# Optimization experiments

Hardware: AMD Instinct MI355X
Metric: run time of the kernel (lower is better)

Reference implementation:

```python
import jax, jax.numpy as jnp
import numpy as np

N = 100000      # nodes
E = 1600000     # edges
F_IN = 64       # num_node_features
R = 8           # num_relations
G = 256         # graphs in batch
H, C = 4, 32    # GAT heads, per-head channels
NEG_SLOPE_ATT = 0.2    # GATConv attention leaky relu
NEG_SLOPE = 0.01       # F.leaky_relu default


def setup_inputs() -> dict:
    key = jax.random.key(0)
    ks = jax.random.split(key, 12)
    init = lambda k, shape, fan: (jax.random.normal(k, shape, jnp.float32) / np.sqrt(fan).astype(np.float32))
    x = jax.random.normal(ks[0], (N, F_IN), jnp.float32)
    edge_index = jax.random.randint(ks[1], (2, E), 0, N)
    edge_type = jax.random.randint(ks[2], (E,), 0, R)
    batch = (jnp.arange(N) * G) // N  # sorted graph ids, every segment non-empty
    return dict(
        x=x, edge_index=edge_index, edge_type=edge_type, batch=batch,
        gat_w=init(ks[3], (F_IN, H * C), F_IN),
        gat_att_src=init(ks[4], (H, C), C),
        gat_att_dst=init(ks[5], (H, C), C),
        gat_bias=jnp.zeros((H * C,), jnp.float32),
        dense1_w=init(ks[6], (H * C, 16), H * C),
        dense1_b=jnp.zeros((16,), jnp.float32),
        rw1=init(ks[7], (R, F_IN, 32), F_IN),
        root1=init(ks[8], (F_IN, 32), F_IN),
        rb1=jnp.zeros((32,), jnp.float32),
        rw2=init(ks[9], (R, 32, 16), 32),
        root2=init(ks[10], (32, 16), 32),
        rb2=jnp.zeros((16,), jnp.float32),
        dense_w=init(ks[11], (32, 1), 32),
        dense_b=jnp.zeros((1,), jnp.float32),
    )


def _gat(x, src, dst, w, att_src, att_dst, bias):
    h = (x @ w).reshape(N, H, C)                       # [N,H,C]
    a_src = jnp.sum(h * att_src, axis=-1)              # [N,H]
    a_dst = jnp.sum(h * att_dst, axis=-1)              # [N,H]
    e = jax.nn.leaky_relu(a_src[src] + a_dst[dst], NEG_SLOPE_ATT)  # [E,H]
    # segment softmax over incoming edges of each dst node
    m = jax.ops.segment_max(e, dst, num_segments=N)    # [N,H]
    p = jnp.exp(e - m[dst])
    s = jax.ops.segment_sum(p, dst, num_segments=N)    # [N,H]
    alpha = p / s[dst]
    msg = h[src] * alpha[:, :, None]                   # [E,H,C]
    out = jax.ops.segment_sum(msg, dst, num_segments=N)
    return out.reshape(N, H * C) + bias


def _rgcn(x, src, dst, edge_type, w, root, bias):
    # per-relation transform of all nodes, then edge gather (PyG RGCNConv, aggr='mean')
    xw = jnp.einsum('ni,rio->rno', x, w)               # [R,N,out]
    msg = xw[edge_type, src]                           # [E,out]
    comb = dst * R + edge_type                         # mean is per (dst, relation)
    cnt = jax.ops.segment_sum(jnp.ones((E,), x.dtype), comb, num_segments=N * R)
    agg = jax.ops.segment_sum(msg / cnt[comb][:, None], dst, num_segments=N)
    return agg + x @ root + bias


def reference(x, edge_index, edge_type, batch, gat_w, gat_att_src, gat_att_dst,
              gat_bias, dense1_w, dense1_b, rw1, root1, rb1, rw2, root2, rb2,
              dense_w, dense_b):
    src, dst = edge_index[0], edge_index[1]
    # GAT branch (dropout treated as identity / eval mode)
    h = _gat(x, src, dst, gat_w, gat_att_src, gat_att_dst, gat_bias)
    h = jax.nn.leaky_relu(h, NEG_SLOPE)
    h = jax.nn.leaky_relu(h @ dense1_w + dense1_b, NEG_SLOPE)
    gmax = jax.ops.segment_max(h, batch, num_segments=G)          # [G,16]
    # RGCN branch
    z = jax.nn.relu(_rgcn(x, src, dst, edge_type, rw1, root1, rb1))
    z = jax.nn.relu(_rgcn(z, src, dst, edge_type, rw2, root2, rb2))
    nodes_per_graph = jax.ops.segment_sum(jnp.ones((N,), x.dtype), batch, num_segments=G)
    gmean = jax.ops.segment_sum(z, batch, num_segments=G) / nodes_per_graph[:, None]
    # fuse
    zc = jnp.concatenate([gmax, gmean], axis=1)                   # [G,32]
    return zc @ dense_w + dense_b                                  # [G,1]
```

## Files before the change

### kernel.cpp

```cpp
#include <hip/hip_runtime.h>
#include <hip/hip_bf16.h>

typedef __hip_bfloat16 bf16;
typedef unsigned short u16;

#define N_NODES 100000
#define N_EDGES 1600000
#define F_IN 64
#define N_REL 8
#define N_GRAPH 256
#define N_HEAD 4
#define HC 128
#define NBLK_SCAN 391

__device__ __forceinline__ float lrelu(float x, float s) { return x >= 0.f ? x : s * x; }
__device__ __forceinline__ unsigned fenc(float f) {
  unsigned b = __float_as_uint(f);
  return (b & 0x80000000u) ? ~b : (b | 0x80000000u);
}
__device__ __forceinline__ float fdec(unsigned u) {
  float v = __uint_as_float((u & 0x80000000u) ? (u & 0x7fffffffu) : ~u);
  return fmaxf(fminf(v, 3e38f), -3e38f);
}
__device__ __forceinline__ float bf2f(bf16 v) { return __bfloat162float(v); }
__device__ __forceinline__ bf16 f2bf(float v) { return __float2bfloat16(v); }
__device__ __forceinline__ float lo_bf(unsigned u) { return __uint_as_float(u << 16); }
__device__ __forceinline__ float hi_bf(unsigned u) { return __uint_as_float(u & 0xFFFF0000u); }
__device__ __forceinline__ unsigned f2bfu(float v) {
  unsigned u = __float_as_uint(v);
  return (u + 0x7FFFu + ((u >> 16) & 1u)) >> 16;
}

template<bool BF> __device__ __forceinline__ float ldf(const void* p, size_t i) {
  if (BF) { u16 v = ((const u16*)p)[i]; return __uint_as_float(((unsigned)v) << 16); }
  else    { return ((const float*)p)[i]; }
}
template<bool BF> __device__ __forceinline__ float2 ldf2(const void* p, size_t i) {
  if (BF) { unsigned v = ((const unsigned*)p)[i]; return make_float2(lo_bf(v), hi_bf(v)); }
  else    { return ((const float2*)p)[i]; }
}

__global__ void k_probe(const u16* __restrict__ xr, int* __restrict__ flag) {
  int t = threadIdx.x;
  int c = 0;
  for (int i = t; i < 1024; i += 256) {
    unsigned e = (xr[i] >> 7) & 0xFFu;
    if (e >= 100u && e <= 140u) c++;
  }
  __shared__ int sc[256];
  sc[t] = c;
  __syncthreads();
  for (int s = 128; s; s >>= 1) { if (t < s) sc[t] += sc[t + s]; __syncthreads(); }
  if (t == 0) *flag = (sc[0] >= 800) ? 1 : 0;
}

template<bool BF>
__device__ __forceinline__ void gat_h_body(const void* x, const void* w, const void* att_s,
                                           const void* att_d, u16* __restrict__ h,
                                           float* __restrict__ a_src, float* __restrict__ a_dst,
                                           int n, float* xs) {
  int j = threadIdx.x;
  if (j < F_IN) xs[j] = ldf<BF>(x, (size_t)n * F_IN + j);
  __syncthreads();
  float acc = 0.f;
#pragma unroll
  for (int k = 0; k < F_IN; ++k) acc += xs[k] * ldf<BF>(w, (size_t)k * HC + j);
  h[(size_t)n * HC + j] = (u16)f2bfu(acc);
  float ps = acc * ldf<BF>(att_s, j);
  float pd = acc * ldf<BF>(att_d, j);
#pragma unroll
  for (int off = 16; off > 0; off >>= 1) {
    ps += __shfl_down(ps, off, 32);
    pd += __shfl_down(pd, off, 32);
  }
  if ((j & 31) == 0) {
    a_src[n * N_HEAD + (j >> 5)] = ps;
    a_dst[n * N_HEAD + (j >> 5)] = pd;
  }
}

__global__ void k_gath_hist(const void* x, const void* w, const void* att_s, const void* att_d,
                            u16* h, float* a_src, float* a_dst,
                            const int* __restrict__ ei, const int* __restrict__ etype,
                            int* __restrict__ deg, int* __restrict__ cnt, const int* flag) {
  __shared__ float xs[F_IN];
  if (blockIdx.x < N_NODES) {
    if (__builtin_amdgcn_readfirstlane(*flag))
      gat_h_body<true>(x, w, att_s, att_d, h, a_src, a_dst, blockIdx.x, xs);
    else
      gat_h_body<false>(x, w, att_s, att_d, h, a_src, a_dst, blockIdx.x, xs);
  } else {
    int e = (blockIdx.x - N_NODES) * 128 + threadIdx.x;
    if (e < N_EDGES) {
      int d = ei[N_EDGES + e], t = etype[e];
      atomicAdd(&deg[d], 1);
      atomicAdd(&cnt[d * N_REL + t], 1);
    }
  }
}

__global__ void k_scan_a(const int* __restrict__ deg, int* __restrict__ rowptr,
                         int* __restrict__ scanblk) {
  __shared__ int buf[256];
  int tid = threadIdx.x;
  int i = blockIdx.x * 256 + tid;
  int v = (i < N_NODES) ? deg[i] : 0;
  buf[tid] = v;
  __syncthreads();
  for (int st = 1; st < 256; st <<= 1) {
    int t = buf[tid];
    int a = (tid >= st) ? buf[tid - st] : 0;
    __syncthreads();
    buf[tid] = t + a;
    __syncthreads();
  }
  if (i < N_NODES) rowptr[i] = buf[tid] - v;
  if (tid == 255) scanblk[blockIdx.x] = buf[255];
}
__global__ void k_scan_b(int* __restrict__ scanblk) {
  __shared__ int buf[512];
  int tid = threadIdx.x;
  int v = (tid < NBLK_SCAN) ? scanblk[tid] : 0;
  buf[tid] = v;
  __syncthreads();
  for (int st = 1; st < 512; st <<= 1) {
    int t = buf[tid];
    int a = (tid >= st) ? buf[tid - st] : 0;
    __syncthreads();
    buf[tid] = t + a;
    __syncthreads();
  }
  if (tid < NBLK_SCAN) scanblk[tid] = buf[tid] - v;
}
__global__ void k_scan_c(int* __restrict__ rowptr, int* __restrict__ wp,
                         const int* __restrict__ scanblk) {
  int i = blockIdx.x * 256 + threadIdx.x;
  if (i < N_NODES) {
    int val = rowptr[i] + scanblk[blockIdx.x];
    rowptr[i] = val;
    wp[i] = val;
  } else if (i == N_NODES) {
    rowptr[N_NODES] = N_EDGES;
  }
}

__global__ void k_scatter(const int* __restrict__ ei, const int* __restrict__ etype,
                          const float* __restrict__ a_src, const float* __restrict__ a_dst,
                          int* __restrict__ wp, unsigned* __restrict__ csr,
                          float4* __restrict__ p_logit, int* __restrict__ dstarr) {
  int e = blockIdx.x * 256 + threadIdx.x;
  if (e >= N_EDGES) return;
  int sn = ei[e], d = ei[N_EDGES + e], t = etype[e];
  int pos = atomicAdd(&wp[d], 1);
  csr[pos] = (unsigned)sn | ((unsigned)t << 20);
  dstarr[pos] = d;
  const float4 as = *(const float4*)&a_src[sn * 4];
  const float4 ad = *(const float4*)&a_dst[d * 4];
  float4 lg;
  lg.x = lrelu(as.x + ad.x, 0.2f);
  lg.y = lrelu(as.y + ad.y, 0.2f);
  lg.z = lrelu(as.z + ad.z, 0.2f);
  lg.w = lrelu(as.w + ad.w, 0.2f);
  p_logit[pos] = lg;
}

__global__ void k_msum(const int* __restrict__ rowptr, const float* __restrict__ p_logit,
                       float* __restrict__ m_arr, float* __restrict__ si_arr) {
  int tid = threadIdx.x;
  int n = blockIdx.x * 16 + (tid >> 4);
  int l16 = tid & 15, head = l16 & 3, slot = l16 >> 2;
  int base = rowptr[n], deg = rowptr[n + 1] - base;
  float m = -1e30f;
  for (int i = slot; i < deg; i += 4) m = fmaxf(m, p_logit[(size_t)(base + i) * 4 + head]);
  m = fmaxf(m, __shfl_xor(m, 4, 64));
  m = fmaxf(m, __shfl_xor(m, 8, 64));
  float s = 0.f;
  for (int i = slot; i < deg; i += 4) s += __expf(p_logit[(size_t)(base + i) * 4 + head] - m);
  s += __shfl_xor(s, 4, 64);
  s += __shfl_xor(s, 8, 64);
  if (slot == 0) {
    m_arr[n * 4 + head] = m;
    si_arr[n * 4 + head] = (deg > 0) ? 1.f / s : 0.f;
  }
}

__global__ void k_alpha(const int* __restrict__ dstarr, const float* __restrict__ m_arr,
                        const float* __restrict__ si_arr, float4* __restrict__ plog4) {
  int p = blockIdx.x * 256 + threadIdx.x;
  if (p >= N_EDGES) return;
  int d = dstarr[p];
  float4 lg = plog4[p];
  const float4 m4 = *(const float4*)&m_arr[d * 4];
  const float4 s4 = *(const float4*)&si_arr[d * 4];
  float4 a;
  a.x = __expf(lg.x - m4.x) * s4.x;
  a.y = __expf(lg.y - m4.y) * s4.y;
  a.z = __expf(lg.z - m4.z) * s4.z;
  a.w = __expf(lg.w - m4.w) * s4.w;
  plog4[p] = a;
}

template<bool BF>
__device__ __forceinline__ void gat_agg_body(const int* __restrict__ rowptr,
                                             const unsigned* __restrict__ csr,
                                             const float* __restrict__ alpha,
                                             const uint2* __restrict__ hu2, const void* gbias,
                                             const void* d1w, const void* d1b,
                                             const int* __restrict__ batch,
                                             unsigned* __restrict__ gmax, int* __restrict__ npg,
                                             float (*os)[132], int bid) {
  int tid = threadIdx.x;
  int wave = tid >> 6, l = tid & 63;
  int d = bid * 4 + wave;
  int base = rowptr[d];
  int deg = rowptr[d + 1] - base;
  int slot = l >> 5, cl = l & 31;
  int head = cl >> 3;
  float a0 = 0.f, a1 = 0.f, a2 = 0.f, a3 = 0.f;
  int i = slot;
  for (; i + 6 < deg; i += 8) {
    unsigned sp0 = csr[base + i],     sp1 = csr[base + i + 2];
    unsigned sp2 = csr[base + i + 4], sp3 = csr[base + i + 6];
    float av0 = alpha[(size_t)(base + i) * 4 + head];
    float av1 = alpha[(size_t)(base + i + 2) * 4 + head];
    float av2 = alpha[(size_t)(base + i + 4) * 4 + head];
    float av3 = alpha[(size_t)(base + i + 6) * 4 + head];
    uint2 h0 = hu2[(size_t)(sp0 & 0xFFFFF) * 32 + cl];
    uint2 h1 = hu2[(size_t)(sp1 & 0xFFFFF) * 32 + cl];
    uint2 h2 = hu2[(size_t)(sp2 & 0xFFFFF) * 32 + cl];
    uint2 h3 = hu2[(size_t)(sp3 & 0xFFFFF) * 32 + cl];
    a0 += lo_bf(h0.x) * av0 + lo_bf(h1.x) * av1 + lo_bf(h2.x) * av2 + lo_bf(h3.x) * av3;
    a1 += hi_bf(h0.x) * av0 + hi_bf(h1.x) * av1 + hi_bf(h2.x) * av2 + hi_bf(h3.x) * av3;
    a2 += lo_bf(h0.y) * av0 + lo_bf(h1.y) * av1 + lo_bf(h2.y) * av2 + lo_bf(h3.y) * av3;
    a3 += hi_bf(h0.y) * av0 + hi_bf(h1.y) * av1 + hi_bf(h2.y) * av2 + hi_bf(h3.y) * av3;
  }
  for (; i < deg; i += 2) {
    unsigned sp = csr[base + i];
    float av = alpha[(size_t)(base + i) * 4 + head];
    uint2 hv = hu2[(size_t)(sp & 0xFFFFF) * 32 + cl];
    a0 += lo_bf(hv.x) * av;
    a1 += hi_bf(hv.x) * av;
    a2 += lo_bf(hv.y) * av;
    a3 += hi_bf(hv.y) * av;
  }
  a0 += __shfl_xor(a0, 32, 64);
  a1 += __shfl_xor(a1, 32, 64);
  a2 += __shfl_xor(a2, 32, 64);
  a3 += __shfl_xor(a3, 32, 64);
  if (slot == 0) {
    os[wave][4 * cl + 0] = lrelu(a0 + ldf<BF>(gbias, 4 * cl + 0), 0.01f);
    os[wave][4 * cl + 1] = lrelu(a1 + ldf<BF>(gbias, 4 * cl + 1), 0.01f);
    os[wave][4 * cl + 2] = lrelu(a2 + ldf<BF>(gbias, 4 * cl + 2), 0.01f);
    os[wave][4 * cl + 3] = lrelu(a3 + ldf<BF>(gbias, 4 * cl + 3), 0.01f);
  }
  __syncthreads();
  if (tid < 64) {
    int node = tid >> 4, out = tid & 15;
    float acc = ldf<BF>(d1b, out);
#pragma unroll
    for (int k = 0; k < HC; ++k) acc += os[node][k] * ldf<BF>(d1w, (size_t)k * 16 + out);
    acc = lrelu(acc, 0.01f);
    atomicMax(&gmax[batch[bid * 4 + node] * 16 + out], fenc(acc));
  }
  if (tid < 4) atomicAdd(&npg[batch[bid * 4 + tid]], 1);
}

template<bool BF>
__device__ __forceinline__ void xw1_body(const void* x, const void* rw1, bf16* __restrict__ xw1,
                                         int n0, int r, float (*xs)[F_IN]) {
  int tid = threadIdx.x;
  for (int i = tid; i < 8 * F_IN; i += 256) {
    int nn = n0 + (i >> 6);
    xs[i >> 6][i & 63] = (nn < N_NODES) ? ldf<BF>(x, (size_t)nn * F_IN + (i & 63)) : 0.f;
  }
  __syncthreads();
  int nl = tid >> 5, c = tid & 31;
  int n = n0 + nl;
  float acc = 0.f;
#pragma unroll
  for (int k = 0; k < F_IN; ++k) acc += xs[nl][k] * ldf<BF>(rw1, (size_t)(r * F_IN + k) * 32 + c);
  if (n < N_NODES) xw1[((size_t)r * N_NODES + n) * 32 + c] = f2bf(acc);
}

__global__ void k_aggxw1(const int* rowptr, const unsigned* csr, const float* alpha,
                         const u16* h, const void* gbias, const void* d1w, const void* d1b,
                         const int* batch, unsigned* gmax, int* npg,
                         const void* x, const void* rw1, bf16* xw1, const int* flag) {
  __shared__ float sh[544];
  int bf = __builtin_amdgcn_readfirstlane(*flag);
  if (blockIdx.x < 25000) {
    if (bf) gat_agg_body<true>(rowptr, csr, alpha, (const uint2*)h, gbias, d1w, d1b,
                               batch, gmax, npg, (float(*)[132])sh, blockIdx.x);
    else    gat_agg_body<false>(rowptr, csr, alpha, (const uint2*)h, gbias, d1w, d1b,
                                batch, gmax, npg, (float(*)[132])sh, blockIdx.x);
  } else {
    int nb = blockIdx.x - 25000;
    int n0 = (nb % 12500) * 8;
    int r  = nb / 12500;
    if (bf) xw1_body<true>(x, rw1, xw1, n0, r, (float(*)[F_IN])sh);
    else    xw1_body<false>(x, rw1, xw1, n0, r, (float(*)[F_IN])sh);
  }
}

template<bool BF>
__device__ __forceinline__ void ragg1_body(const int* __restrict__ rowptr,
                                           const unsigned* __restrict__ csr,
                                           const int* __restrict__ cnt,
                                           const unsigned* __restrict__ xw, const void* x,
                                           const void* root1, const void* rb1,
                                           float* __restrict__ z1) {
  __shared__ float xs[4][F_IN];
  __shared__ float cinv[4][N_REL];
  int tid = threadIdx.x;
  int n0 = blockIdx.x * 4;
  {
    int nn = n0 + (tid >> 6);
    xs[tid >> 6][tid & 63] = ldf<BF>(x, (size_t)nn * F_IN + (tid & 63));
  }
  if (tid < 32) {
    int cv = cnt[(n0 + (tid >> 3)) * N_REL + (tid & 7)];
    cinv[tid >> 3][tid & 7] = (cv > 0) ? 1.f / (float)cv : 0.f;
  }
  __syncthreads();
  int wave = tid >> 6, l = tid & 63;
  int slot = l >> 4, cl = l & 15;
  int n = n0 + wave;
  int base = rowptr[n], deg = rowptr[n + 1] - base;
  float a0 = 0.f, a1 = 0.f;
  int i = slot;
  for (; i + 4 < deg; i += 8) {
    unsigned sp0 = csr[base + i], sp1 = csr[base + i + 4];
    int t0 = sp0 >> 20, t1 = sp1 >> 20;
    unsigned v0 = xw[((size_t)t0 * N_NODES + (sp0 & 0xFFFFF)) * 16 + cl];
    unsigned v1 = xw[((size_t)t1 * N_NODES + (sp1 & 0xFFFFF)) * 16 + cl];
    float c0 = cinv[wave][t0], c1 = cinv[wave][t1];
    a0 += lo_bf(v0) * c0 + lo_bf(v1) * c1;
    a1 += hi_bf(v0) * c0 + hi_bf(v1) * c1;
  }
  if (i < deg) {
    unsigned sp = csr[base + i];
    int t = sp >> 20;
    unsigned v = xw[((size_t)t * N_NODES + (sp & 0xFFFFF)) * 16 + cl];
    float c0 = cinv[wave][t];
    a0 += lo_bf(v) * c0;
    a1 += hi_bf(v) * c0;
  }
#pragma unroll
  for (int kk = 0; kk < 16; ++kk) {
    int k = slot * 16 + kk;
    float xv = xs[wave][k];
    float2 wv = ldf2<BF>(root1, (size_t)k * 16 + cl);
    a0 += xv * wv.x;
    a1 += xv * wv.y;
  }
  a0 += __shfl_xor(a0, 16, 64); a0 += __shfl_xor(a0, 32, 64);
  a1 += __shfl_xor(a1, 16, 64); a1 += __shfl_xor(a1, 32, 64);
  if (slot == 0) {
    z1[(size_t)n * 32 + 2 * cl]     = fmaxf(a0 + ldf<BF>(rb1, 2 * cl), 0.f);
    z1[(size_t)n * 32 + 2 * cl + 1] = fmaxf(a1 + ldf<BF>(rb1, 2 * cl + 1), 0.f);
  }
}
__global__ void k_ragg1(const int* rowptr, const unsigned* csr, const int* cnt,
                        const bf16* xw1, const void* x, const void* root1, const void* rb1,
                        float* z1, const int* flag) {
  if (__builtin_amdgcn_readfirstlane(*flag))
    ragg1_body<true>(rowptr, csr, cnt, (const unsigned*)xw1, x, root1, rb1, z1);
  else
    ragg1_body<false>(rowptr, csr, cnt, (const unsigned*)xw1, x, root1, rb1, z1);
}

template<bool BF>
__device__ __forceinline__ void zw2_body(const float* __restrict__ z1, const void* rw2,
                                         bf16* __restrict__ zw2) {
  __shared__ float zs[16][32];
  int tid = threadIdx.x;
  int n0 = blockIdx.x * 16;
  for (int i = tid; i < 16 * 32; i += 256) {
    int nn = n0 + (i >> 5);
    zs[i >> 5][i & 31] = (nn < N_NODES) ? z1[(size_t)nn * 32 + (i & 31)] : 0.f;
  }
  __syncthreads();
  int nl = tid >> 4, c = tid & 15;
  int n = n0 + nl, r = blockIdx.y;
  float acc = 0.f;
#pragma unroll
  for (int k = 0; k < 32; ++k) acc += zs[nl][k] * ldf<BF>(rw2, (size_t)(r * 32 + k) * 16 + c);
  if (n < N_NODES) zw2[((size_t)r * N_NODES + n) * 16 + c] = f2bf(acc);
}
__global__ void k_zw2(const float* z1, const void* rw2, bf16* zw2, const int* flag) {
  if (__builtin_amdgcn_readfirstlane(*flag)) zw2_body<true>(z1, rw2, zw2);
  else zw2_body<false>(z1, rw2, zw2);
}

template<bool BF>
__device__ __forceinline__ void ragg2_body(const int* __restrict__ rowptr,
                                           const unsigned* __restrict__ csr,
                                           const int* __restrict__ cnt,
                                           const unsigned* __restrict__ zw,
                                           const float* __restrict__ z1, const void* root2,
                                           const void* rb2, const int* __restrict__ batch,
                                           float* __restrict__ gsum) {
  __shared__ float zs[4][33];
  __shared__ float cinv[4][N_REL];
  int tid = threadIdx.x;
  int n0 = blockIdx.x * 4;
  if (tid < 128) {
    int nn = n0 + (tid >> 5);
    zs[tid >> 5][tid & 31] = z1[(size_t)nn * 32 + (tid & 31)];
  }
  if (tid < 32) {
    int cv = cnt[(n0 + (tid >> 3)) * N_REL + (tid & 7)];
    cinv[tid >> 3][tid & 7] = (cv > 0) ? 1.f / (float)cv : 0.f;
  }
  __syncthreads();
  int wave = tid >> 6, l = tid & 63;
  int slot = l >> 3, cl = l & 7;
  int n = n0 + wave;
  int base = rowptr[n], deg = rowptr[n + 1] - base;
  float a0 = 0.f, a1 = 0.f;
  int i = slot;
  for (; i + 8 < deg; i += 16) {
    unsigned sp0 = csr[base + i], sp1 = csr[base + i + 8];
    int t0 = sp0 >> 20, t1 = sp1 >> 20;
    unsigned v0 = zw[((size_t)t0 * N_NODES + (sp0 & 0xFFFFF)) * 8 + cl];
    unsigned v1 = zw[((size_t)t1 * N_NODES + (sp1 & 0xFFFFF)) * 8 + cl];
    float c0 = cinv[wave][t0], c1 = cinv[wave][t1];
    a0 += lo_bf(v0) * c0 + lo_bf(v1) * c1;
    a1 += hi_bf(v0) * c0 + hi_bf(v1) * c1;
  }
  if (i < deg) {
    unsigned sp = csr[base + i];
    int t = sp >> 20;
    unsigned v = zw[((size_t)t * N_NODES + (sp & 0xFFFFF)) * 8 + cl];
    float c0 = cinv[wave][t];
    a0 += lo_bf(v) * c0;
    a1 += hi_bf(v) * c0;
  }
#pragma unroll
  for (int kk = 0; kk < 4; ++kk) {
    int k = slot * 4 + kk;
    float zv = zs[wave][k];
    float2 wv = ldf2<BF>(root2, (size_t)k * 8 + cl);
    a0 += zv * wv.x;
    a1 += zv * wv.y;
  }
  a0 += __shfl_xor(a0, 8, 64); a0 += __shfl_xor(a0, 16, 64); a0 += __shfl_xor(a0, 32, 64);
  a1 += __shfl_xor(a1, 8, 64); a1 += __shfl_xor(a1, 16, 64); a1 += __shfl_xor(a1, 32, 64);
  if (slot == 0) {
    float z2a = fmaxf(a0 + ldf<BF>(rb2, 2 * cl), 0.f);
    float z2b = fmaxf(a1 + ldf<BF>(rb2, 2 * cl + 1), 0.f);
    int g = batch[n];
    atomicAdd(&gsum[g * 16 + 2 * cl], z2a);
    atomicAdd(&gsum[g * 16 + 2 * cl + 1], z2b);
  }
}
__global__ void k_ragg2(const int* rowptr, const unsigned* csr, const int* cnt,
                        const bf16* zw2, const float* z1, const void* root2, const void* rb2,
                        const int* batch, float* gsum, const int* flag) {
  if (__builtin_amdgcn_readfirstlane(*flag))
    ragg2_body<true>(rowptr, csr, cnt, (const unsigned*)zw2, z1, root2, rb2, batch, gsum);
  else
    ragg2_body<false>(rowptr, csr, cnt, (const unsigned*)zw2, z1, root2, rb2, batch, gsum);
}

template<bool BF>
__device__ __forceinline__ void final_body(const unsigned* __restrict__ gmax,
                                           const float* __restrict__ gsum,
                                           const int* __restrict__ npg, const void* dw,
                                           const void* db, void* out) {
  int g = threadIdx.x;
  if (g >= N_GRAPH) return;
  float acc = ldf<BF>(db, 0);
  int np = npg[g]; if (np < 1) np = 1;
  float inv = 1.f / (float)np;
#pragma unroll
  for (int c = 0; c < 16; ++c) {
    acc += fdec(gmax[g * 16 + c]) * ldf<BF>(dw, c);
    acc += (gsum[g * 16 + c] * inv) * ldf<BF>(dw, 16 + c);
  }
  if (BF) ((bf16*)out)[g] = f2bf(acc);
  else ((float*)out)[g] = acc;
}
__global__ void k_final(const unsigned* gmax, const float* gsum, const int* npg,
                        const void* dw, const void* db, void* out, const int* flag) {
  if (__builtin_amdgcn_readfirstlane(*flag)) final_body<true>(gmax, gsum, npg, dw, db, out);
  else final_body<false>(gmax, gsum, npg, dw, db, out);
}

extern "C" void kernel_launch(void* const* d_in, const int* in_sizes, int n_in,
                              void* d_out, int out_size, void* d_ws, size_t ws_size,
                              hipStream_t stream) {
  const void* x        = d_in[0];
  const int*  ei       = (const int*)d_in[1];
  const int*  etype    = (const int*)d_in[2];
  const int*  batch    = (const int*)d_in[3];
  const void* gat_w    = d_in[4];
  const void* att_src  = d_in[5];
  const void* att_dst  = d_in[6];
  const void* gat_bias = d_in[7];
  const void* d1w      = d_in[8];
  const void* d1b      = d_in[9];
  const void* rw1      = d_in[10];
  const void* root1    = d_in[11];
  const void* rb1      = d_in[12];
  const void* rw2      = d_in[13];
  const void* root2    = d_in[14];
  const void* rb2      = d_in[15];
  const void* dw       = d_in[16];
  const void* db       = d_in[17];

  char* ws = (char*)d_ws;
  const size_t o_h     = 0;
  const size_t o_plog  = 25600000;
  const size_t o_xw1   = 51200000;
  const size_t o_dst   = 51200000;
  const size_t o_zw2   = 0;
  const size_t o_asrc  = 102400000;
  const size_t o_adst  = 104000000;
  const size_t o_deg   = 105600000;
  const size_t o_rowp  = 106000000;
  const size_t o_wp    = 106400016;
  const size_t o_cnt   = 106800016;
  const size_t o_csr   = 110000016;
  const size_t o_z1    = 116400016;
  const size_t o_sblk  = 129200016;
  const size_t o_gmax  = 129201600;
  const size_t o_gsum  = 129217984;
  const size_t o_npg   = 129234368;
  const size_t o_flag  = 129235392;
  const size_t total   = 129235396;
  if (ws_size < total) return;

  u16*      h      = (u16*)(ws + o_h);
  float*    plog   = (float*)(ws + o_plog);
  bf16*     xw1    = (bf16*)(ws + o_xw1);
  int*      dstarr = (int*)(ws + o_dst);
  bf16*     zw2    = (bf16*)(ws + o_zw2);
  float*    a_src  = (float*)(ws + o_asrc);
  float*    a_dst  = (float*)(ws + o_adst);
  int*      deg    = (int*)(ws + o_deg);
  int*      rowptr = (int*)(ws + o_rowp);
  int*      wp     = (int*)(ws + o_wp);
  int*      cnt    = (int*)(ws + o_cnt);
  unsigned* csr    = (unsigned*)(ws + o_csr);
  float*    z1     = (float*)(ws + o_z1);
  int*      sblk   = (int*)(ws + o_sblk);
  unsigned* gmax   = (unsigned*)(ws + o_gmax);
  float*    gsum   = (float*)(ws + o_gsum);
  int*      npg    = (int*)(ws + o_npg);
  int*      flag   = (int*)(ws + o_flag);

  k_probe<<<1, 256, 0, stream>>>((const u16*)x, flag);

  hipMemsetAsync(ws + o_deg, 0, o_csr - o_deg, stream);
  hipMemsetAsync(ws + o_gmax, 0, 33792, stream);

  k_gath_hist<<<N_NODES + 12500, 128, 0, stream>>>(x, gat_w, att_src, att_dst, h, a_src, a_dst,
                                                   ei, etype, deg, cnt, flag);

  k_scan_a<<<NBLK_SCAN, 256, 0, stream>>>(deg, rowptr, sblk);
  k_scan_b<<<1, 512, 0, stream>>>(sblk);
  k_scan_c<<<NBLK_SCAN, 256, 0, stream>>>(rowptr, wp, sblk);
  k_scatter<<<(N_EDGES + 255) / 256, 256, 0, stream>>>(ei, etype, a_src, a_dst, wp, csr,
                                                       (float4*)plog, dstarr);

  k_msum<<<N_NODES / 16, 256, 0, stream>>>(rowptr, plog, a_src, a_dst);
  k_alpha<<<(N_EDGES + 255) / 256, 256, 0, stream>>>(dstarr, a_src, a_dst, (float4*)plog);

  k_aggxw1<<<25000 + 100000, 256, 0, stream>>>(rowptr, csr, plog, h, gat_bias, d1w, d1b,
                                               batch, gmax, npg, x, rw1, xw1, flag);

  k_ragg1<<<N_NODES / 4, 256, 0, stream>>>(rowptr, csr, cnt, xw1, x, root1, rb1, z1, flag);

  k_zw2<<<dim3((N_NODES + 15) / 16, N_REL), 256, 0, stream>>>(z1, rw2, zw2, flag);
  k_ragg2<<<N_NODES / 4, 256, 0, stream>>>(rowptr, csr, cnt, zw2, z1, root2, rb2,
                                           batch, gsum, flag);

  k_final<<<1, 256, 0, stream>>>(gmax, gsum, npg, dw, db, d_out, flag);
}
```

Baseline: 1.232 ms.

## Fuse softmax into GAT aggregation and register-tile node transforms

The per-edge max/sum and alpha kernels are removed. Each wave now computes the segment max and inverse sum itself and applies exp on the fly while aggregating, which drops the dstarr array and a full pass over the logits. The GAT and x·rw1 transforms are register-tiled so each block handles 16 nodes with weights held in registers, and they are launched alongside the degree histogram. The RGCN layer-1 aggregation is merged into the GAT aggregation launch. The cost is that logits are read twice more inside the aggregation and each edge's exp is recomputed per channel lane.

```diff
diff --git a/kernel.cpp b/kernel.cpp
--- a/kernel.cpp
+++ b/kernel.cpp
@@ -55,47 +55,106 @@
 }
 
 template<bool BF>
-__device__ __forceinline__ void gat_h_body(const void* x, const void* w, const void* att_s,
-                                           const void* att_d, u16* __restrict__ h,
-                                           float* __restrict__ a_src, float* __restrict__ a_dst,
-                                           int n, float* xs) {
-  int j = threadIdx.x;
-  if (j < F_IN) xs[j] = ldf<BF>(x, (size_t)n * F_IN + j);
-  __syncthreads();
-  float acc = 0.f;
-#pragma unroll
-  for (int k = 0; k < F_IN; ++k) acc += xs[k] * ldf<BF>(w, (size_t)k * HC + j);
-  h[(size_t)n * HC + j] = (u16)f2bfu(acc);
-  float ps = acc * ldf<BF>(att_s, j);
-  float pd = acc * ldf<BF>(att_d, j);
-#pragma unroll
-  for (int off = 16; off > 0; off >>= 1) {
-    ps += __shfl_down(ps, off, 32);
-    pd += __shfl_down(pd, off, 32);
-  }
-  if ((j & 31) == 0) {
-    a_src[n * N_HEAD + (j >> 5)] = ps;
-    a_dst[n * N_HEAD + (j >> 5)] = pd;
-  }
-}
-
-__global__ void k_gath_hist(const void* x, const void* w, const void* att_s, const void* att_d,
-                            u16* h, float* a_src, float* a_dst,
-                            const int* __restrict__ ei, const int* __restrict__ etype,
-                            int* __restrict__ deg, int* __restrict__ cnt, const int* flag) {
-  __shared__ float xs[F_IN];
-  if (blockIdx.x < N_NODES) {
+__device__ __forceinline__ void gat_body(const void* x, const void* w, const void* att_s,
+                                         const void* att_d, u16* __restrict__ h,
+                                         float* __restrict__ a_src, float* __restrict__ a_dst,
+                                         int n0, float* xs) {
+  int tid = threadIdx.x;
+  for (int i = tid; i < 16 * F_IN; i += 256)
+    xs[i] = ldf<BF>(x, (size_t)(n0 + (i >> 6)) * F_IN + (i & 63));
+  __syncthreads();
+  int g = tid >> 7, c = tid & 127;
+  float as_c = ldf<BF>(att_s, c), ad_c = ldf<BF>(att_d, c);
+  float acc[8] = {0.f, 0.f, 0.f, 0.f, 0.f, 0.f, 0.f, 0.f};
+  for (int kh = 0; kh < F_IN; kh += 32) {
+    float wreg[32];
+#pragma unroll
+    for (int j = 0; j < 32; ++j) wreg[j] = ldf<BF>(w, (size_t)(kh + j) * HC + c);
+#pragma unroll
+    for (int n = 0; n < 8; ++n) {
+      const float* xr = &xs[(g * 8 + n) * F_IN + kh];
+#pragma unroll
+      for (int j = 0; j < 32; j += 4) {
+        float4 xv = *(const float4*)&xr[j];
+        acc[n] += xv.x * wreg[j];
+        acc[n] += xv.y * wreg[j + 1];
+        acc[n] += xv.z * wreg[j + 2];
+        acc[n] += xv.w * wreg[j + 3];
+      }
+    }
+  }
+  int l = tid & 63, head = c >> 5;
+#pragma unroll
+  for (int n = 0; n < 8; ++n) {
+    int node = n0 + g * 8 + n;
+    h[(size_t)node * HC + c] = (u16)f2bfu(acc[n]);
+    float ps = acc[n] * as_c, pd = acc[n] * ad_c;
+#pragma unroll
+    for (int off = 16; off > 0; off >>= 1) {
+      ps += __shfl_xor(ps, off, 64);
+      pd += __shfl_xor(pd, off, 64);
+    }
+    if ((l & 31) == 0) {
+      a_src[node * N_HEAD + head] = ps;
+      a_dst[node * N_HEAD + head] = pd;
+    }
+  }
+}
+
+template<bool BF>
+__device__ __forceinline__ void xw1_body(const void* x, const void* rw1, bf16* __restrict__ xw1,
+                                         int n0, float* xs) {
+  int tid = threadIdx.x;
+  for (int i = tid; i < 16 * F_IN; i += 256)
+    xs[i] = ldf<BF>(x, (size_t)(n0 + (i >> 6)) * F_IN + (i & 63));
+  __syncthreads();
+  int r = tid >> 5, c = tid & 31;
+  float acc[16] = {0.f, 0.f, 0.f, 0.f, 0.f, 0.f, 0.f, 0.f,
+                   0.f, 0.f, 0.f, 0.f, 0.f, 0.f, 0.f, 0.f};
+  for (int kh = 0; kh < F_IN; kh += 32) {
+    float wreg[32];
+#pragma unroll
+    for (int j = 0; j < 32; ++j)
+      wreg[j] = ldf<BF>(rw1, (size_t)(r * F_IN + kh + j) * 32 + c);
+#pragma unroll
+    for (int n = 0; n < 16; ++n) {
+      const float* xr = &xs[n * F_IN + kh];
+#pragma unroll
+      for (int j = 0; j < 32; j += 4) {
+        float4 xv = *(const float4*)&xr[j];
+        acc[n] += xv.x * wreg[j];
+        acc[n] += xv.y * wreg[j + 1];
+        acc[n] += xv.z * wreg[j + 2];
+        acc[n] += xv.w * wreg[j + 3];
+      }
+    }
+  }
+#pragma unroll
+  for (int n = 0; n < 16; ++n)
+    xw1[((size_t)r * N_NODES + (n0 + n)) * 32 + c] = f2bf(acc[n]);
+}
+
+__global__ void k_gxh(const void* x, const void* w, const void* att_s, const void* att_d,
+                      u16* h, float* a_src, float* a_dst, const void* rw1, bf16* xw1,
+                      const int* __restrict__ ei, const int* __restrict__ etype,
+                      int* __restrict__ deg, int* __restrict__ cnt, const int* flag) {
+  __shared__ __align__(16) float xs[16 * F_IN];
+  int bid = blockIdx.x;
+  if (bid < 6250) {
+    int e = bid * 256 + threadIdx.x;
+    int d = ei[N_EDGES + e], t = etype[e];
+    atomicAdd(&deg[d], 1);
+    atomicAdd(&cnt[d * N_REL + t], 1);
+  } else if (bid < 12500) {
+    int n0 = (bid - 6250) * 16;
     if (__builtin_amdgcn_readfirstlane(*flag))
-      gat_h_body<true>(x, w, att_s, att_d, h, a_src, a_dst, blockIdx.x, xs);
+      gat_body<true>(x, w, att_s, att_d, h, a_src, a_dst, n0, xs);
     else
-      gat_h_body<false>(x, w, att_s, att_d, h, a_src, a_dst, blockIdx.x, xs);
+      gat_body<false>(x, w, att_s, att_d, h, a_src, a_dst, n0, xs);
   } else {
-    int e = (blockIdx.x - N_NODES) * 128 + threadIdx.x;
-    if (e < N_EDGES) {
-      int d = ei[N_EDGES + e], t = etype[e];
-      atomicAdd(&deg[d], 1);
-      atomicAdd(&cnt[d * N_REL + t], 1);
-    }
+    int n0 = (bid - 12500) * 16;
+    if (__builtin_amdgcn_readfirstlane(*flag)) xw1_body<true>(x, rw1, xw1, n0, xs);
+    else xw1_body<false>(x, rw1, xw1, n0, xs);
   }
 }
 
@@ -147,13 +206,12 @@
 __global__ void k_scatter(const int* __restrict__ ei, const int* __restrict__ etype,
                           const float* __restrict__ a_src, const float* __restrict__ a_dst,
                           int* __restrict__ wp, unsigned* __restrict__ csr,
-                          float4* __restrict__ p_logit, int* __restrict__ dstarr) {
+                          float4* __restrict__ p_logit) {
   int e = blockIdx.x * 256 + threadIdx.x;
   if (e >= N_EDGES) return;
   int sn = ei[e], d = ei[N_EDGES + e], t = etype[e];
   int pos = atomicAdd(&wp[d], 1);
   csr[pos] = (unsigned)sn | ((unsigned)t << 20);
-  dstarr[pos] = d;
   const float4 as = *(const float4*)&a_src[sn * 4];
   const float4 ad = *(const float4*)&a_dst[d * 4];
   float4 lg;
@@ -164,67 +222,49 @@
   p_logit[pos] = lg;
 }
 
-__global__ void k_msum(const int* __restrict__ rowptr, const float* __restrict__ p_logit,
-                       float* __restrict__ m_arr, float* __restrict__ si_arr) {
-  int tid = threadIdx.x;
-  int n = blockIdx.x * 16 + (tid >> 4);
-  int l16 = tid & 15, head = l16 & 3, slot = l16 >> 2;
-  int base = rowptr[n], deg = rowptr[n + 1] - base;
-  float m = -1e30f;
-  for (int i = slot; i < deg; i += 4) m = fmaxf(m, p_logit[(size_t)(base + i) * 4 + head]);
-  m = fmaxf(m, __shfl_xor(m, 4, 64));
-  m = fmaxf(m, __shfl_xor(m, 8, 64));
-  float s = 0.f;
-  for (int i = slot; i < deg; i += 4) s += __expf(p_logit[(size_t)(base + i) * 4 + head] - m);
-  s += __shfl_xor(s, 4, 64);
-  s += __shfl_xor(s, 8, 64);
-  if (slot == 0) {
-    m_arr[n * 4 + head] = m;
-    si_arr[n * 4 + head] = (deg > 0) ? 1.f / s : 0.f;
-  }
-}
-
-__global__ void k_alpha(const int* __restrict__ dstarr, const float* __restrict__ m_arr,
-                        const float* __restrict__ si_arr, float4* __restrict__ plog4) {
-  int p = blockIdx.x * 256 + threadIdx.x;
-  if (p >= N_EDGES) return;
-  int d = dstarr[p];
-  float4 lg = plog4[p];
-  const float4 m4 = *(const float4*)&m_arr[d * 4];
-  const float4 s4 = *(const float4*)&si_arr[d * 4];
-  float4 a;
-  a.x = __expf(lg.x - m4.x) * s4.x;
-  a.y = __expf(lg.y - m4.y) * s4.y;
-  a.z = __expf(lg.z - m4.z) * s4.z;
-  a.w = __expf(lg.w - m4.w) * s4.w;
-  plog4[p] = a;
-}
-
-template<bool BF>
-__device__ __forceinline__ void gat_agg_body(const int* __restrict__ rowptr,
-                                             const unsigned* __restrict__ csr,
-                                             const float* __restrict__ alpha,
-                                             const uint2* __restrict__ hu2, const void* gbias,
-                                             const void* d1w, const void* d1b,
-                                             const int* __restrict__ batch,
-                                             unsigned* __restrict__ gmax, int* __restrict__ npg,
-                                             float (*os)[132], int bid) {
+template<bool BF>
+__device__ __forceinline__ void agg_body(const int* __restrict__ rowptr,
+                                         const unsigned* __restrict__ csr,
+                                         const float* __restrict__ plog,
+                                         const uint2* __restrict__ hu2, const void* gbias,
+                                         const void* d1w, const void* d1b,
+                                         const int* __restrict__ batch,
+                                         unsigned* __restrict__ gmax, int* __restrict__ npg,
+                                         float (*os)[132], int bid) {
   int tid = threadIdx.x;
   int wave = tid >> 6, l = tid & 63;
   int d = bid * 4 + wave;
   int base = rowptr[d];
   int deg = rowptr[d + 1] - base;
+  float m = -1e30f, si;
+  {
+    int hd = l & 3, sl = l >> 2;
+    for (int i = sl; i < deg; i += 16) m = fmaxf(m, plog[(size_t)(base + i) * 4 + hd]);
+    m = fmaxf(m, __shfl_xor(m, 4, 64));
+    m = fmaxf(m, __shfl_xor(m, 8, 64));
+    m = fmaxf(m, __shfl_xor(m, 16, 64));
+    m = fmaxf(m, __shfl_xor(m, 32, 64));
+    float s = 0.f;
+    for (int i = sl; i < deg; i += 16) s += __expf(plog[(size_t)(base + i) * 4 + hd] - m);
+    s += __shfl_xor(s, 4, 64);
+    s += __shfl_xor(s, 8, 64);
+    s += __shfl_xor(s, 16, 64);
+    s += __shfl_xor(s, 32, 64);
+    si = (deg > 0) ? 1.f / s : 0.f;
+  }
   int slot = l >> 5, cl = l & 31;
   int head = cl >> 3;
+  float mh = __shfl(m, head, 64);
+  float sih = __shfl(si, head, 64);
   float a0 = 0.f, a1 = 0.f, a2 = 0.f, a3 = 0.f;
   int i = slot;
   for (; i + 6 < deg; i += 8) {
     unsigned sp0 = csr[base + i],     sp1 = csr[base + i + 2];
     unsigned sp2 = csr[base + i + 4], sp3 = csr[base + i + 6];
-    float av0 = alpha[(size_t)(base + i) * 4 + head];
-    float av1 = alpha[(size_t)(base + i + 2) * 4 + head];
-    float av2 = alpha[(size_t)(base + i + 4) * 4 + head];
-    float av3 = alpha[(size_t)(base + i + 6) * 4 + head];
+    float av0 = __expf(plog[(size_t)(base + i) * 4 + head] - mh) * sih;
+    float av1 = __expf(plog[(size_t)(base + i + 2) * 4 + head] - mh) * sih;
+    float av2 = __expf(plog[(size_t)(base + i + 4) * 4 + head] - mh) * sih;
+    float av3 = __expf(plog[(size_t)(base + i + 6) * 4 + head] - mh) * sih;
     uint2 h0 = hu2[(size_t)(sp0 & 0xFFFFF) * 32 + cl];
     uint2 h1 = hu2[(size_t)(sp1 & 0xFFFFF) * 32 + cl];
     uint2 h2 = hu2[(size_t)(sp2 & 0xFFFFF) * 32 + cl];
@@ -236,7 +276,7 @@
   }
   for (; i < deg; i += 2) {
     unsigned sp = csr[base + i];
-    float av = alpha[(size_t)(base + i) * 4 + head];
+    float av = __expf(plog[(size_t)(base + i) * 4 + head] - mh) * sih;
     uint2 hv = hu2[(size_t)(sp & 0xFFFFF) * 32 + cl];
     a0 += lo_bf(hv.x) * av;
     a1 += hi_bf(hv.x) * av;
@@ -266,53 +306,16 @@
 }
 
 template<bool BF>
-__device__ __forceinline__ void xw1_body(const void* x, const void* rw1, bf16* __restrict__ xw1,
-                                         int n0, int r, float (*xs)[F_IN]) {
-  int tid = threadIdx.x;
-  for (int i = tid; i < 8 * F_IN; i += 256) {
-    int nn = n0 + (i >> 6);
-    xs[i >> 6][i & 63] = (nn < N_NODES) ? ldf<BF>(x, (size_t)nn * F_IN + (i & 63)) : 0.f;
-  }
-  __syncthreads();
-  int nl = tid >> 5, c = tid & 31;
-  int n = n0 + nl;
-  float acc = 0.f;
-#pragma unroll
-  for (int k = 0; k < F_IN; ++k) acc += xs[nl][k] * ldf<BF>(rw1, (size_t)(r * F_IN + k) * 32 + c);
-  if (n < N_NODES) xw1[((size_t)r * N_NODES + n) * 32 + c] = f2bf(acc);
-}
-
-__global__ void k_aggxw1(const int* rowptr, const unsigned* csr, const float* alpha,
-                         const u16* h, const void* gbias, const void* d1w, const void* d1b,
-                         const int* batch, unsigned* gmax, int* npg,
-                         const void* x, const void* rw1, bf16* xw1, const int* flag) {
-  __shared__ float sh[544];
-  int bf = __builtin_amdgcn_readfirstlane(*flag);
-  if (blockIdx.x < 25000) {
-    if (bf) gat_agg_body<true>(rowptr, csr, alpha, (const uint2*)h, gbias, d1w, d1b,
-                               batch, gmax, npg, (float(*)[132])sh, blockIdx.x);
-    else    gat_agg_body<false>(rowptr, csr, alpha, (const uint2*)h, gbias, d1w, d1b,
-                                batch, gmax, npg, (float(*)[132])sh, blockIdx.x);
-  } else {
-    int nb = blockIdx.x - 25000;
-    int n0 = (nb % 12500) * 8;
-    int r  = nb / 12500;
-    if (bf) xw1_body<true>(x, rw1, xw1, n0, r, (float(*)[F_IN])sh);
-    else    xw1_body<false>(x, rw1, xw1, n0, r, (float(*)[F_IN])sh);
-  }
-}
-
-template<bool BF>
 __device__ __forceinline__ void ragg1_body(const int* __restrict__ rowptr,
                                            const unsigned* __restrict__ csr,
                                            const int* __restrict__ cnt,
                                            const unsigned* __restrict__ xw, const void* x,
                                            const void* root1, const void* rb1,
-                                           float* __restrict__ z1) {
-  __shared__ float xs[4][F_IN];
-  __shared__ float cinv[4][N_REL];
-  int tid = threadIdx.x;
-  int n0 = blockIdx.x * 4;
+                                           float* __restrict__ z1, float* sh, int bid) {
+  float (*xs)[F_IN] = (float(*)[F_IN])sh;
+  float (*cinv)[N_REL] = (float(*)[N_REL])(sh + 4 * F_IN);
+  int tid = threadIdx.x;
+  int n0 = bid * 4;
   {
     int nn = n0 + (tid >> 6);
     xs[tid >> 6][tid & 63] = ldf<BF>(x, (size_t)nn * F_IN + (tid & 63));
@@ -360,13 +363,25 @@
     z1[(size_t)n * 32 + 2 * cl + 1] = fmaxf(a1 + ldf<BF>(rb1, 2 * cl + 1), 0.f);
   }
 }
-__global__ void k_ragg1(const int* rowptr, const unsigned* csr, const int* cnt,
-                        const bf16* xw1, const void* x, const void* root1, const void* rb1,
-                        float* z1, const int* flag) {
-  if (__builtin_amdgcn_readfirstlane(*flag))
-    ragg1_body<true>(rowptr, csr, cnt, (const unsigned*)xw1, x, root1, rb1, z1);
-  else
-    ragg1_body<false>(rowptr, csr, cnt, (const unsigned*)xw1, x, root1, rb1, z1);
+
+__global__ void k_aggragg1(const int* rowptr, const unsigned* csr, const float* plog,
+                           const u16* h, const void* gbias, const void* d1w, const void* d1b,
+                           const int* batch, unsigned* gmax, int* npg,
+                           const int* cnt, const bf16* xw1, const void* x,
+                           const void* root1, const void* rb1, float* z1, const int* flag) {
+  __shared__ __align__(16) float sh[544];
+  int bf = __builtin_amdgcn_readfirstlane(*flag);
+  if (blockIdx.x < 25000) {
+    if (bf) agg_body<true>(rowptr, csr, plog, (const uint2*)h, gbias, d1w, d1b,
+                           batch, gmax, npg, (float(*)[132])sh, blockIdx.x);
+    else    agg_body<false>(rowptr, csr, plog, (const uint2*)h, gbias, d1w, d1b,
+                            batch, gmax, npg, (float(*)[132])sh, blockIdx.x);
+  } else {
+    if (bf) ragg1_body<true>(rowptr, csr, cnt, (const unsigned*)xw1, x, root1, rb1, z1,
+                             sh, blockIdx.x - 25000);
+    else    ragg1_body<false>(rowptr, csr, cnt, (const unsigned*)xw1, x, root1, rb1, z1,
+                              sh, blockIdx.x - 25000);
+  }
 }
 
 template<bool BF>
@@ -513,7 +528,6 @@
   const size_t o_h     = 0;
   const size_t o_plog  = 25600000;
   const size_t o_xw1   = 51200000;
-  const size_t o_dst   = 51200000;
   const size_t o_zw2   = 0;
   const size_t o_asrc  = 102400000;
   const size_t o_adst  = 104000000;
@@ -534,7 +548,6 @@
   u16*      h      = (u16*)(ws + o_h);
   float*    plog   = (float*)(ws + o_plog);
   bf16*     xw1    = (bf16*)(ws + o_xw1);
-  int*      dstarr = (int*)(ws + o_dst);
   bf16*     zw2    = (bf16*)(ws + o_zw2);
   float*    a_src  = (float*)(ws + o_asrc);
   float*    a_dst  = (float*)(ws + o_adst);
@@ -555,22 +568,17 @@
   hipMemsetAsync(ws + o_deg, 0, o_csr - o_deg, stream);
   hipMemsetAsync(ws + o_gmax, 0, 33792, stream);
 
-  k_gath_hist<<<N_NODES + 12500, 128, 0, stream>>>(x, gat_w, att_src, att_dst, h, a_src, a_dst,
-                                                   ei, etype, deg, cnt, flag);
+  k_gxh<<<18750, 256, 0, stream>>>(x, gat_w, att_src, att_dst, h, a_src, a_dst,
+                                   rw1, xw1, ei, etype, deg, cnt, flag);
 
   k_scan_a<<<NBLK_SCAN, 256, 0, stream>>>(deg, rowptr, sblk);
   k_scan_b<<<1, 512, 0, stream>>>(sblk);
   k_scan_c<<<NBLK_SCAN, 256, 0, stream>>>(rowptr, wp, sblk);
   k_scatter<<<(N_EDGES + 255) / 256, 256, 0, stream>>>(ei, etype, a_src, a_dst, wp, csr,
-                                                       (float4*)plog, dstarr);
-
-  k_msum<<<N_NODES / 16, 256, 0, stream>>>(rowptr, plog, a_src, a_dst);
-  k_alpha<<<(N_EDGES + 255) / 256, 256, 0, stream>>>(dstarr, a_src, a_dst, (float4*)plog);
-
-  k_aggxw1<<<25000 + 100000, 256, 0, stream>>>(rowptr, csr, plog, h, gat_bias, d1w, d1b,
-                                               batch, gmax, npg, x, rw1, xw1, flag);
-
-  k_ragg1<<<N_NODES / 4, 256, 0, stream>>>(rowptr, csr, cnt, xw1, x, root1, rb1, z1, flag);
+                                                       (float4*)plog);
+
+  k_aggragg1<<<50000, 256, 0, stream>>>(rowptr, csr, plog, h, gat_bias, d1w, d1b,
+                                        batch, gmax, npg, cnt, xw1, x, root1, rb1, z1, flag);
 
   k_zw2<<<dim3((N_NODES + 15) / 16, N_REL), 256, 0, stream>>>(z1, rw2, zw2, flag);
   k_ragg2<<<N_NODES / 4, 256, 0, stream>>>(rowptr, csr, cnt, zw2, z1, root2, rb2,
```

Result: slower. 2.092 ms (+69.8%).
